# Performance work log

Hardware: AMD Instinct MI355X
Metric: run time of the kernel (lower is better)

Reference implementation:

```python
import jax, jax.numpy as jnp
import numpy as np

EMB = 512
HEADS = 8

def setup_inputs() -> dict:
    key = jax.random.key(0)
    ks = jax.random.split(key, 6)
    x = jax.random.normal(ks[0], (8, 1024, EMB), dtype=jnp.float32)
    s = EMB ** -0.5
    Wq = jax.random.normal(ks[1], (EMB, EMB), dtype=jnp.float32) * s
    Wk = jax.random.normal(ks[2], (EMB, EMB), dtype=jnp.float32) * s
    Wv = jax.random.normal(ks[3], (EMB, EMB), dtype=jnp.float32) * s
    ln_gamma = jnp.ones((EMB,), dtype=jnp.float32)
    ln_beta = jnp.zeros((EMB,), dtype=jnp.float32)
    return {"x": x, "Wq": Wq, "Wk": Wk, "Wv": Wv, "ln_gamma": ln_gamma, "ln_beta": ln_beta}

def reference(x, Wq, Wk, Wv, ln_gamma, ln_beta):
    B, S, E = x.shape
    H = HEADS
    D = E // H
    scale = E ** -0.5  # note: source scales by emb_size**-0.5, not head_dim
    # projections (bias=False, torch Linear: x @ W.T)
    q = (x @ Wq.T).reshape(B, S, H, D).transpose(0, 2, 1, 3)  # [B,H,S,D]
    k = (x @ Wk.T).reshape(B, S, H, D).transpose(0, 2, 1, 3)
    v = (x @ Wv.T).reshape(B, S, H, D).transpose(0, 2, 1, 3)
    attn = jnp.einsum('bhqd,bhkd->bhqk', q, k) * scale
    attn = jax.nn.softmax(attn, axis=-1)
    out = jnp.einsum('bhqk,bhkd->bhqd', attn, v)
    out = out.transpose(0, 2, 1, 3).reshape(B, S, E)
    # LayerNorm (eps=1e-5, torch default)
    mu = jnp.mean(out, axis=-1, keepdims=True)
    var = jnp.var(out, axis=-1, keepdims=True)
    out = (out - mu) * jax.lax.rsqrt(var + 1e-5) * ln_gamma + ln_beta
    return out
```

## Files before the change

kernel.cpp:

```cpp
#include <hip/hip_runtime.h>
#include <hip/hip_bf16.h>

typedef __bf16 bf16_t;
typedef __bf16 bf16x4 __attribute__((ext_vector_type(4)));
typedef __bf16 bf16x8 __attribute__((ext_vector_type(8)));
typedef float  f32x4  __attribute__((ext_vector_type(4)));
typedef short  short4v __attribute__((ext_vector_type(4)));

#define GLL(gp, lp) __builtin_amdgcn_global_load_lds((const __attribute__((address_space(1))) void*)(gp), (__attribute__((address_space(3))) void*)(lp), 16, 0, 0)

__device__ __forceinline__ f32x4 mfma16x16x16_bf16(bf16x4 a, bf16x4 b, f32x4 c) {
#if __has_builtin(__builtin_amdgcn_mfma_f32_16x16x16_bf16)
    return __builtin_amdgcn_mfma_f32_16x16x16_bf16(a, b, c, 0, 0, 0);
#else
    return __builtin_amdgcn_mfma_f32_16x16x16bf16_1k(__builtin_bit_cast(short4v, a), __builtin_bit_cast(short4v, b), c, 0, 0, 0);
#endif
}

__device__ __forceinline__ float fexp2(float x) {
#if __has_builtin(__builtin_amdgcn_exp2f)
    return __builtin_amdgcn_exp2f(x);
#else
    return exp2f(x);
#endif
}

__global__ __launch_bounds__(256) void cvt_kernel(const float* __restrict__ x,
                                                  const float* __restrict__ wq,
                                                  const float* __restrict__ wk,
                                                  const float* __restrict__ wv,
                                                  bf16_t* __restrict__ xb,
                                                  bf16_t* __restrict__ wall) {
    const int TOT4 = 1245184;
    for (int i = blockIdx.x * blockDim.x + threadIdx.x; i < TOT4; i += gridDim.x * blockDim.x) {
        const float* src; bf16_t* dst; int off;
        if (i < 1048576) { src = x; dst = xb; off = i; }
        else {
            int j = i - 1048576;
            int wsel = j >> 16;
            off = j & 65535;
            src = (wsel == 0) ? wq : ((wsel == 1) ? wk : wv);
            dst = wall + ((size_t)wsel << 18);
        }
        float4 v = *(const float4*)(src + (size_t)off * 4);
        bf16x4 o = { (bf16_t)v.x, (bf16_t)v.y, (bf16_t)v.z, (bf16_t)v.w };
        *(bf16x4*)(dst + (size_t)off * 4) = o;
    }
}

__global__ __launch_bounds__(256) void proj_kernel(const bf16_t* __restrict__ xb,
                                                   const bf16_t* __restrict__ wall,
                                                   bf16_t* __restrict__ Qb,
                                                   bf16_t* __restrict__ Kb,
                                                   bf16_t* __restrict__ Vt) {
    __shared__ char psm[34816];

    const int tid = threadIdx.x;
    const int w = tid >> 6, lane = tid & 63;
    const int bx = blockIdx.x;
    const int nb = bx % 12, mb = bx / 12;
    const int n0 = nb * 128, m0 = mb * 128;
    const int wn = w & 1, wm = w >> 1;
    const int l15 = lane & 15, g = lane >> 4;

    const int srow = w * 32 + (lane >> 2);
    const int kcol = (lane & 3) * 8;
    const bf16_t* wsrc0 = wall + (size_t)(n0 + srow) * 512 + kcol;
    const bf16_t* xsrc0 = xb + (size_t)(m0 + srow) * 512 + kcol;

    f32x4 acc[4][4] = {};

    {
        bf16_t* lw = (bf16_t*)(psm) + w * 1024;
        bf16_t* lx = (bf16_t*)(psm + 8192) + w * 1024;
        GLL(wsrc0, lw);
        GLL(wsrc0 + 8192, lw + 512);
        GLL(xsrc0, lx);
        GLL(xsrc0 + 8192, lx + 512);
    }
    __syncthreads();

    for (int kt = 0; kt < 16; ++kt) {
        const int buf = kt & 1;
        if (kt < 15) {
            const int ko = (kt + 1) * 32;
            bf16_t* lw = (bf16_t*)(psm + (buf ^ 1) * 16384) + w * 1024;
            bf16_t* lx = (bf16_t*)(psm + (buf ^ 1) * 16384 + 8192) + w * 1024;
            GLL(wsrc0 + ko, lw);
            GLL(wsrc0 + 8192 + ko, lw + 512);
            GLL(xsrc0 + ko, lx);
            GLL(xsrc0 + 8192 + ko, lx + 512);
        }
        const bf16_t* sW = (const bf16_t*)(psm + buf * 16384);
        const bf16_t* sX = (const bf16_t*)(psm + buf * 16384 + 8192);

        bf16x8 af[4], bfv[4];
#pragma unroll
        for (int ni = 0; ni < 4; ++ni)
            af[ni] = *(const bf16x8*)(sW + (wn * 64 + ni * 16 + l15) * 32 + g * 8);
#pragma unroll
        for (int mi = 0; mi < 4; ++mi)
            bfv[mi] = *(const bf16x8*)(sX + (wm * 64 + mi * 16 + l15) * 32 + g * 8);
#pragma unroll
        for (int ni = 0; ni < 4; ++ni)
#pragma unroll
            for (int mi = 0; mi < 4; ++mi)
                acc[ni][mi] = __builtin_amdgcn_mfma_f32_16x16x32_bf16(af[ni], bfv[mi], acc[ni][mi], 0, 0, 0);
        __syncthreads();
    }

    const int which = n0 >> 9;
    if (which < 2) {
        bf16_t* dst = (which == 0) ? Qb : Kb;
#pragma unroll
        for (int ni = 0; ni < 4; ++ni) {
#pragma unroll
            for (int mi = 0; mi < 4; ++mi) {
                int j = (n0 & 511) + wn * 64 + ni * 16 + g * 4;
                int h = j >> 6, dd = j & 63;
                int sb = m0 + wm * 64 + mi * 16 + l15;
                int b = sb >> 10, s = sb & 1023;
                bf16x4 o = { (bf16_t)acc[ni][mi][0], (bf16_t)acc[ni][mi][1],
                             (bf16_t)acc[ni][mi][2], (bf16_t)acc[ni][mi][3] };
                *(bf16x4*)(dst + ((size_t)((b * 8 + h) * 1024 + s)) * 64 + dd) = o;
            }
        }
    } else {
        bf16_t* ctile = (bf16_t*)psm;
#pragma unroll
        for (int ni = 0; ni < 4; ++ni)
#pragma unroll
            for (int mi = 0; mi < 4; ++mi)
#pragma unroll
                for (int r = 0; r < 4; ++r)
                    ctile[(wn * 64 + ni * 16 + g * 4 + r) * 136 + wm * 64 + mi * 16 + l15] =
                        (bf16_t)acc[ni][mi][r];
        __syncthreads();
        const int rr = tid >> 1, half = tid & 1;
        const int jv = (n0 & 511) + rr;
        const int hh = jv >> 6, dd = jv & 63;
        const int b = m0 >> 10, sb = (m0 & 1023) + half * 64;
        bf16_t* dst = Vt + ((size_t)((b * 8 + hh) * 64 + dd)) * 1024 + sb;
        const bf16_t* src = ctile + rr * 136 + half * 64;
#pragma unroll
        for (int u = 0; u < 8; ++u)
            *(bf16x8*)(dst + u * 8) = *(const bf16x8*)(src + u * 8);
    }
}

__global__ __launch_bounds__(512, 2) void attn_kernel(const bf16_t* __restrict__ Qb,
                                                      const bf16_t* __restrict__ Kb,
                                                      const bf16_t* __restrict__ Vt,
                                                      bf16_t* __restrict__ Ob) {
    __shared__ char smem[65536];
    const int tid = threadIdx.x;
    const int w = tid >> 6, lane = tid & 63;
    const int pipe = w >> 2, ws = w & 3;
    const int l15 = lane & 15, g = lane >> 4, l7 = lane & 7;

    const int bx = blockIdx.x;
    const int head = (bx & 7) * 8 + ((bx >> 3) & 7);
    const int qq = bx >> 6;
    const int q0 = qq * 256 + ws * 64;

    const size_t hoff = (size_t)head << 16;
    const bf16_t* Qh = Qb + hoff;
    const char* Kh = (const char*)(Kb + hoff) + pipe * 65536;
    const char* Vh = (const char*)(Vt + hoff) + pipe * 1024;

    const float c2 = 0.06376390597f;

    bf16x8 qf[4][2];
#pragma unroll
    for (int qh = 0; qh < 4; ++qh) {
        const bf16_t* qp = Qh + (q0 + qh * 16 + l15) * 64 + g * 8;
        bf16x8 a = *(const bf16x8*)(qp);
        bf16x8 bq = *(const bf16x8*)(qp + 32);
#pragma unroll
        for (int j = 0; j < 8; ++j) {
            a[j] = (bf16_t)((float)a[j] * c2);
            bq[j] = (bf16_t)((float)bq[j] * c2);
        }
        qf[qh][0] = a; qf[qh][1] = bq;
    }

    const int srow = ws * 8 + (lane >> 3);
    const int sw16 = (l7 ^ ((lane >> 3) & 7)) << 4;
    const char* Ksrc = Kh + srow * 128 + sw16;
    const char* Vsrc = Vh + srow * 2048 + sw16;
    char* region = smem + pipe * 32768;
    char* dstK = region + ws * 1024;
    char* dstV = region + 8192 + ws * 1024;

    const int e0 = (l7 ^ g) << 4;
    const int f0 = (g << 3) ^ (l7 << 4);

    f32x4 oacc[4][4] = {};
    f32x4 dacc[4] = {};
    const bf16x4 ones = { (bf16_t)1.0f, (bf16_t)1.0f, (bf16_t)1.0f, (bf16_t)1.0f };
    const f32x4 minit = { -4.0f, -4.0f, -4.0f, -4.0f };

    GLL(Ksrc, dstK);
    GLL(Ksrc + 4096, dstK + 4096);
    GLL(Vsrc, dstV);
    GLL(Vsrc + 65536, dstV + 4096);
    __syncthreads();

    for (int c = 0; c < 8; ++c) {
        const int buf = c & 1;
        if (c < 7) {
            const int nbo = (buf ^ 1) * 16384;
            GLL(Ksrc + (c + 1) * 8192, dstK + nbo);
            GLL(Ksrc + (c + 1) * 8192 + 4096, dstK + nbo + 4096);
            GLL(Vsrc + (c + 1) * 128, dstV + nbo);
            GLL(Vsrc + (c + 1) * 128 + 65536, dstV + nbo + 4096);
        }
        const char* bK = region + buf * 16384;
        const char* bV = bK + 8192;

#pragma unroll
        for (int sub = 0; sub < 4; ++sub) {
            const char* rowp = bK + (sub * 16 + l15) * 128;
            bf16x8 ka0 = *(const bf16x8*)(rowp + e0);
            bf16x8 ka1 = *(const bf16x8*)(rowp + (e0 ^ 64));
            bf16x4 pb[4];
#pragma unroll
            for (int qh = 0; qh < 4; ++qh) {
                f32x4 st = __builtin_amdgcn_mfma_f32_16x16x32_bf16(ka0, qf[qh][0], minit, 0, 0, 0);
                st = __builtin_amdgcn_mfma_f32_16x16x32_bf16(ka1, qf[qh][1], st, 0, 0, 0);
                bf16x4 pv = { (bf16_t)fexp2(st[0]), (bf16_t)fexp2(st[1]),
                              (bf16_t)fexp2(st[2]), (bf16_t)fexp2(st[3]) };
                pb[qh] = pv;
                dacc[qh] = mfma16x16x16_bf16(ones, pv, dacc[qh]);
            }
#pragma unroll
            for (int dt = 0; dt < 4; ++dt) {
                bf16x4 va = *(const bf16x4*)(bV + (dt * 16 + l15) * 128 + (f0 ^ (sub << 5)));
                oacc[0][dt] = mfma16x16x16_bf16(va, pb[0], oacc[0][dt]);
                oacc[1][dt] = mfma16x16x16_bf16(va, pb[1], oacc[1][dt]);
                oacc[2][dt] = mfma16x16x16_bf16(va, pb[2], oacc[2][dt]);
                oacc[3][dt] = mfma16x16x16_bf16(va, pb[3], oacc[3][dt]);
            }
        }
        __syncthreads();
    }

    const int b = head >> 3, h = head & 7;
#pragma unroll
    for (int r = 0; r < 2; ++r) {
        if (pipe == 1) {
#pragma unroll
            for (int j = 0; j < 2; ++j) {
                const int qh = r * 2 + j;
#pragma unroll
                for (int dt = 0; dt < 4; ++dt)
                    *(f32x4*)(smem + ws * 8192 + j * 4096 + dt * 1024 + lane * 16) = oacc[qh][dt];
                *(float*)(smem + 32768 + (ws * 2 + j) * 256 + lane * 4) = dacc[qh][0];
            }
        }
        __syncthreads();
        if (pipe == 0) {
#pragma unroll
            for (int j = 0; j < 2; ++j) {
                const int qh = r * 2 + j;
                const float dn = dacc[qh][0] + *(const float*)(smem + 32768 + (ws * 2 + j) * 256 + lane * 4);
                const float inv = 1.0f / dn;
                const int s = q0 + qh * 16 + l15;
                bf16_t* op = Ob + ((size_t)(b * 1024 + s)) * 512 + h * 64 + g * 4;
#pragma unroll
                for (int dt = 0; dt < 4; ++dt) {
                    f32x4 t = oacc[qh][dt] + *(const f32x4*)(smem + ws * 8192 + j * 4096 + dt * 1024 + lane * 16);
                    bf16x4 o = { (bf16_t)(t[0] * inv), (bf16_t)(t[1] * inv),
                                 (bf16_t)(t[2] * inv), (bf16_t)(t[3] * inv) };
                    *(bf16x4*)(op + dt * 16) = o;
                }
            }
        }
        __syncthreads();
    }
}

__global__ __launch_bounds__(256) void ln_kernel(const bf16_t* __restrict__ O,
                                                 const float* __restrict__ gamma,
                                                 const float* __restrict__ beta,
                                                 float* __restrict__ out) {
    const int w = threadIdx.x >> 6, lane = threadIdx.x & 63;
    const int row = blockIdx.x * 4 + w;
    const bf16_t* rp = O + (size_t)row * 512 + lane * 8;
    bf16x8 v8 = *(const bf16x8*)rp;
    float v[8];
    float sum = 0.0f, sq = 0.0f;
#pragma unroll
    for (int i = 0; i < 8; ++i) { v[i] = (float)v8[i]; sum += v[i]; sq += v[i] * v[i]; }
#pragma unroll
    for (int msk = 1; msk < 64; msk <<= 1) {
        sum += __shfl_xor(sum, msk);
        sq  += __shfl_xor(sq, msk);
    }
    const float mean = sum * (1.0f / 512.0f);
    const float var = sq * (1.0f / 512.0f) - mean * mean;
    const float rs = rsqrtf(var + 1e-5f);
    float4 g0 = *(const float4*)(gamma + lane * 8);
    float4 g1 = *(const float4*)(gamma + lane * 8 + 4);
    float4 b0 = *(const float4*)(beta + lane * 8);
    float4 b1 = *(const float4*)(beta + lane * 8 + 4);
    float* op = out + (size_t)row * 512 + lane * 8;
    float4 o0, o1;
    o0.x = (v[0] - mean) * rs * g0.x + b0.x;
    o0.y = (v[1] - mean) * rs * g0.y + b0.y;
    o0.z = (v[2] - mean) * rs * g0.z + b0.z;
    o0.w = (v[3] - mean) * rs * g0.w + b0.w;
    o1.x = (v[4] - mean) * rs * g1.x + b1.x;
    o1.y = (v[5] - mean) * rs * g1.y + b1.y;
    o1.z = (v[6] - mean) * rs * g1.z + b1.z;
    o1.w = (v[7] - mean) * rs * g1.w + b1.w;
    *(float4*)op = o0;
    *(float4*)(op + 4) = o1;
}

extern "C" void kernel_launch(void* const* d_in, const int* in_sizes, int n_in,
                              void* d_out, int out_size, void* d_ws, size_t ws_size,
                              hipStream_t stream) {
    const float* x  = (const float*)d_in[0];
    const float* wq = (const float*)d_in[1];
    const float* wk = (const float*)d_in[2];
    const float* wv = (const float*)d_in[3];
    const float* gamma = (const float*)d_in[4];
    const float* beta  = (const float*)d_in[5];
    float* out = (float*)d_out;

    char* ws = (char*)d_ws;
    bf16_t* xb   = (bf16_t*)(ws);
    bf16_t* wall = (bf16_t*)(ws + 8388608);
    bf16_t* Qb   = (bf16_t*)(ws + 9961472);
    bf16_t* Kb   = (bf16_t*)(ws + 18350080);
    bf16_t* Vt   = (bf16_t*)(ws + 26738688);
    bf16_t* Ob   = (bf16_t*)(ws + 35127296);

    hipLaunchKernelGGL(cvt_kernel,  dim3(1024), dim3(256), 0, stream, x, wq, wk, wv, xb, wall);
    hipLaunchKernelGGL(proj_kernel, dim3(768),  dim3(256), 0, stream, xb, wall, Qb, Kb, Vt);
    hipLaunchKernelGGL(attn_kernel, dim3(256),  dim3(512), 0, stream, Qb, Kb, Vt, Ob);
    hipLaunchKernelGGL(ln_kernel,   dim3(2048), dim3(256), 0, stream, Ob, gamma, beta, out);
}
```

Measured before the change: 65.77 us.

## Restructure attention kernel to stage half of K/V in 128KB LDS per phase

Drops the two-pipe split of the key range, which needed an LDS reduction of partial outputs and denominators at the end. Each of 8 waves now owns 32 queries and walks all 1024 keys. K and V for half the keys (64KB each) are bulk-loaded into LDS per phase, replacing the per-chunk double-buffered pipeline. This removes the cross-pipe reduction and the per-chunk barriers, but there is no overlap between loading the second half and compute. The 128KB of LDS per block also likely limits occupancy to one block per CU, down from the launch-bound target of two, and each wave gets less work per K/V load.

```diff
diff --git a/kernel.cpp b/kernel.cpp
--- a/kernel.cpp
+++ b/kernel.cpp
@@ -152,27 +152,37 @@
                                                       const bf16_t* __restrict__ Kb,
                                                       const bf16_t* __restrict__ Vt,
                                                       bf16_t* __restrict__ Ob) {
-    __shared__ char smem[65536];
+    __shared__ char smK[65536];
+    __shared__ char smV[65536];
     const int tid = threadIdx.x;
     const int w = tid >> 6, lane = tid & 63;
-    const int pipe = w >> 2, ws = w & 3;
     const int l15 = lane & 15, g = lane >> 4, l7 = lane & 7;
 
     const int bx = blockIdx.x;
-    const int head = (bx & 7) * 8 + ((bx >> 3) & 7);
+    const int head = bx & 63;
     const int qq = bx >> 6;
-    const int q0 = qq * 256 + ws * 64;
+    const int q0 = qq * 256 + w * 32;
 
     const size_t hoff = (size_t)head << 16;
     const bf16_t* Qh = Qb + hoff;
-    const char* Kh = (const char*)(Kb + hoff) + pipe * 65536;
-    const char* Vh = (const char*)(Vt + hoff) + pipe * 1024;
+    const char* Kh = (const char*)(Kb + hoff);
+    const char* Vh = (const char*)(Vt + hoff);
 
     const float c2 = 0.06376390597f;
 
-    bf16x8 qf[4][2];
-#pragma unroll
-    for (int qh = 0; qh < 4; ++qh) {
+    const char* KsrcT = Kh + (tid >> 3) * 128 + (((tid & 7) ^ ((tid >> 3) & 7)) << 4);
+    const char* VsrcT = Vh + (size_t)w * 2048 + ((lane ^ w) << 4);
+    char* KdstT = smK + (w << 10);
+    char* VdstT = smV + (w << 10);
+
+#pragma unroll
+    for (int c = 0; c < 8; ++c) GLL(KsrcT + c * 8192, KdstT + c * 8192);
+#pragma unroll
+    for (int c = 0; c < 8; ++c) GLL(VsrcT + c * 16384, VdstT + c * 8192);
+
+    bf16x8 qf[2][2];
+#pragma unroll
+    for (int qh = 0; qh < 2; ++qh) {
         const bf16_t* qp = Qh + (q0 + qh * 16 + l15) * 64 + g * 8;
         bf16x8 a = *(const bf16x8*)(qp);
         bf16x8 bq = *(const bf16x8*)(qp + 32);
@@ -184,48 +194,25 @@
         qf[qh][0] = a; qf[qh][1] = bq;
     }
 
-    const int srow = ws * 8 + (lane >> 3);
-    const int sw16 = (l7 ^ ((lane >> 3) & 7)) << 4;
-    const char* Ksrc = Kh + srow * 128 + sw16;
-    const char* Vsrc = Vh + srow * 2048 + sw16;
-    char* region = smem + pipe * 32768;
-    char* dstK = region + ws * 1024;
-    char* dstV = region + 8192 + ws * 1024;
-
-    const int e0 = (l7 ^ g) << 4;
-    const int f0 = (g << 3) ^ (l7 << 4);
-
-    f32x4 oacc[4][4] = {};
-    f32x4 dacc[4] = {};
+    f32x4 oacc[2][4] = {};
+    f32x4 dacc[2] = {};
     const bf16x4 ones = { (bf16_t)1.0f, (bf16_t)1.0f, (bf16_t)1.0f, (bf16_t)1.0f };
     const f32x4 minit = { -4.0f, -4.0f, -4.0f, -4.0f };
 
-    GLL(Ksrc, dstK);
-    GLL(Ksrc + 4096, dstK + 4096);
-    GLL(Vsrc, dstV);
-    GLL(Vsrc + 65536, dstV + 4096);
+    const int ke0 = (g ^ l7) << 4;
+
     __syncthreads();
 
-    for (int c = 0; c < 8; ++c) {
-        const int buf = c & 1;
-        if (c < 7) {
-            const int nbo = (buf ^ 1) * 16384;
-            GLL(Ksrc + (c + 1) * 8192, dstK + nbo);
-            GLL(Ksrc + (c + 1) * 8192 + 4096, dstK + nbo + 4096);
-            GLL(Vsrc + (c + 1) * 128, dstV + nbo);
-            GLL(Vsrc + (c + 1) * 128 + 65536, dstV + nbo + 4096);
-        }
-        const char* bK = region + buf * 16384;
-        const char* bV = bK + 8192;
-
-#pragma unroll
-        for (int sub = 0; sub < 4; ++sub) {
-            const char* rowp = bK + (sub * 16 + l15) * 128;
-            bf16x8 ka0 = *(const bf16x8*)(rowp + e0);
-            bf16x8 ka1 = *(const bf16x8*)(rowp + (e0 ^ 64));
-            bf16x4 pb[4];
-#pragma unroll
-            for (int qh = 0; qh < 4; ++qh) {
+#pragma unroll 1
+    for (int phase = 0; phase < 2; ++phase) {
+#pragma unroll 2
+        for (int sub = 0; sub < 32; ++sub) {
+            const char* krp = smK + (sub * 16 + l15) * 128;
+            bf16x8 ka0 = *(const bf16x8*)(krp + ke0);
+            bf16x8 ka1 = *(const bf16x8*)(krp + (ke0 ^ 64));
+            bf16x4 pb[2];
+#pragma unroll
+            for (int qh = 0; qh < 2; ++qh) {
                 f32x4 st = __builtin_amdgcn_mfma_f32_16x16x32_bf16(ka0, qf[qh][0], minit, 0, 0, 0);
                 st = __builtin_amdgcn_mfma_f32_16x16x32_bf16(ka1, qf[qh][1], st, 0, 0, 0);
                 bf16x4 pv = { (bf16_t)fexp2(st[0]), (bf16_t)fexp2(st[1]),
@@ -233,50 +220,36 @@
                 pb[qh] = pv;
                 dacc[qh] = mfma16x16x16_bf16(ones, pv, dacc[qh]);
             }
+            const int vcol = (((sub * 2 + (g >> 1)) ^ l7) << 4) + ((g & 1) << 3);
 #pragma unroll
             for (int dt = 0; dt < 4; ++dt) {
-                bf16x4 va = *(const bf16x4*)(bV + (dt * 16 + l15) * 128 + (f0 ^ (sub << 5)));
+                bf16x4 va = *(const bf16x4*)(smV + (dt * 16 + l15) * 1024 + vcol);
                 oacc[0][dt] = mfma16x16x16_bf16(va, pb[0], oacc[0][dt]);
                 oacc[1][dt] = mfma16x16x16_bf16(va, pb[1], oacc[1][dt]);
-                oacc[2][dt] = mfma16x16x16_bf16(va, pb[2], oacc[2][dt]);
-                oacc[3][dt] = mfma16x16x16_bf16(va, pb[3], oacc[3][dt]);
             }
         }
-        __syncthreads();
+        if (phase == 0) {
+            __syncthreads();
+#pragma unroll
+            for (int c = 0; c < 8; ++c) GLL(KsrcT + 65536 + c * 8192, KdstT + c * 8192);
+#pragma unroll
+            for (int c = 0; c < 8; ++c) GLL(VsrcT + 1024 + c * 16384, VdstT + c * 8192);
+            __syncthreads();
+        }
     }
 
     const int b = head >> 3, h = head & 7;
 #pragma unroll
-    for (int r = 0; r < 2; ++r) {
-        if (pipe == 1) {
-#pragma unroll
-            for (int j = 0; j < 2; ++j) {
-                const int qh = r * 2 + j;
-#pragma unroll
-                for (int dt = 0; dt < 4; ++dt)
-                    *(f32x4*)(smem + ws * 8192 + j * 4096 + dt * 1024 + lane * 16) = oacc[qh][dt];
-                *(float*)(smem + 32768 + (ws * 2 + j) * 256 + lane * 4) = dacc[qh][0];
-            }
-        }
-        __syncthreads();
-        if (pipe == 0) {
-#pragma unroll
-            for (int j = 0; j < 2; ++j) {
-                const int qh = r * 2 + j;
-                const float dn = dacc[qh][0] + *(const float*)(smem + 32768 + (ws * 2 + j) * 256 + lane * 4);
-                const float inv = 1.0f / dn;
-                const int s = q0 + qh * 16 + l15;
-                bf16_t* op = Ob + ((size_t)(b * 1024 + s)) * 512 + h * 64 + g * 4;
-#pragma unroll
-                for (int dt = 0; dt < 4; ++dt) {
-                    f32x4 t = oacc[qh][dt] + *(const f32x4*)(smem + ws * 8192 + j * 4096 + dt * 1024 + lane * 16);
-                    bf16x4 o = { (bf16_t)(t[0] * inv), (bf16_t)(t[1] * inv),
-                                 (bf16_t)(t[2] * inv), (bf16_t)(t[3] * inv) };
-                    *(bf16x4*)(op + dt * 16) = o;
-                }
-            }
-        }
-        __syncthreads();
+    for (int qh = 0; qh < 2; ++qh) {
+        const float inv = 1.0f / dacc[qh][0];
+        const int s = q0 + qh * 16 + l15;
+        bf16_t* op = Ob + ((size_t)(b * 1024 + s)) * 512 + h * 64 + g * 4;
+#pragma unroll
+        for (int dt = 0; dt < 4; ++dt) {
+            bf16x4 o = { (bf16_t)(oacc[qh][dt][0] * inv), (bf16_t)(oacc[qh][dt][1] * inv),
+                         (bf16_t)(oacc[qh][dt][2] * inv), (bf16_t)(oacc[qh][dt][3] * inv) };
+            *(bf16x4*)(op + dt * 16) = o;
+        }
     }
 }
 
```

Result: no change. 65.92 us (+0.2%).
